# Kernel tuning notes

Hardware: AMD Instinct MI355X
Metric: run time of the kernel (lower is better)

Reference implementation:

```python
import jax, jax.numpy as jnp
import numpy as np

HEADS = 8
DIM_HEAD = 32
SCALE = DIM_HEAD ** -0.5
EPS = 1e-5


def setup_inputs() -> dict:
    key = jax.random.key(0)
    k1, k2, k3 = jax.random.split(key, 3)
    b, dim, n = 8, 512, 8192
    hidden = HEADS * DIM_HEAD  # 256
    return {
        "x": jax.random.normal(k1, (b, dim, n), dtype=jnp.float32),
        "g": jnp.ones((1, dim, 1), dtype=jnp.float32),
        "b_ln": jnp.zeros((1, dim, 1), dtype=jnp.float32),
        "w_qkv": jax.random.normal(k2, (hidden * 3, dim), dtype=jnp.float32) * (dim ** -0.5),
        "w_out": jax.random.normal(k3, (dim, hidden), dtype=jnp.float32) * (hidden ** -0.5),
        "b_out": jnp.zeros((dim,), dtype=jnp.float32),
    }


def reference(x, g, b_ln, w_qkv, w_out, b_out):
    b, c, n = x.shape
    # channel LayerNorm (biased variance over dim=1)
    mean = jnp.mean(x, axis=1, keepdims=True)
    var = jnp.var(x, axis=1, keepdims=True)
    x_norm = (x - mean) / jnp.sqrt(var + EPS) * g + b_ln
    # 1x1 conv QKV projection: [3*hidden, c] x [b, c, n] -> [b, 3*hidden, n]
    qkv = jnp.einsum('oc,bcn->bon', w_qkv, x_norm)
    hidden = w_qkv.shape[0] // 3
    q, k, v = jnp.split(qkv, 3, axis=1)
    # [b, h, dh, n]
    q = q.reshape(b, HEADS, DIM_HEAD, n) * SCALE
    k = k.reshape(b, HEADS, DIM_HEAD, n)
    v = v.reshape(b, HEADS, DIM_HEAD, n)
    k = jax.nn.softmax(k, axis=-1)  # softmax over sequence positions
    # linear attention: context = k v^T  (dh x dh per head), then context q
    context = jnp.einsum('bhdn,bhen->bhde', k, v)
    out = jnp.einsum('bhde,bhdn->bhen', context, q)
    out = out.reshape(b, hidden, n)
    out = jnp.einsum('oc,bcn->bon', w_out, out) + b_out[None, :, None]
    return out + x
```

## Files before the change

kernel.cpp:

```cpp
#include <hip/hip_runtime.h>
#include <hip/hip_bf16.h>
#include <math.h>

#define HEADS 8
#define DH 32
#define BATCH 8
#define CDIM 512
#define NSEQ 8192
#define HID 256
#define O3 768
#define LNEPS 1e-5f
#define QSCALE 0.1767766952966369f

typedef __bf16 bf16x8 __attribute__((ext_vector_type(8)));
typedef float f32x4 __attribute__((ext_vector_type(4)));
typedef unsigned short u16;
typedef u16 u16x4 __attribute__((ext_vector_type(4)));
typedef u16 u16x8 __attribute__((ext_vector_type(8)));

__device__ __forceinline__ void gld_lds16(const void* g, void* l) {
  __builtin_amdgcn_global_load_lds(
      (const __attribute__((address_space(1))) unsigned int*)g,
      (__attribute__((address_space(3))) unsigned int*)l, 16, 0, 0);
}

__device__ __forceinline__ float ldx(const void* p, size_t i, bool f32) {
  if (f32) {
    float v = ((const float*)p)[i];
    return __builtin_isfinite(v) ? v : 0.f;
  }
  return __bfloat162float(((const __hip_bfloat16*)p)[i]);
}

__device__ __forceinline__ u16 b16(float v) {
  union { __hip_bfloat16 h; u16 u; } cv;
  cv.h = __float2bfloat16(v);
  return cv.u;
}

__device__ __forceinline__ float fb16(u16 u) {
  return __uint_as_float((unsigned)u << 16);
}

__device__ __forceinline__ void stage8(__hip_bfloat16* dst, const void* src, size_t idx, bool f32) {
  if (f32) {
    const float* s = (const float*)src + idx;
#pragma unroll
    for (int t = 0; t < 8; ++t) {
      float v = s[t];
      if (!__builtin_isfinite(v)) v = 0.f;
      dst[t] = __float2bfloat16(v);
    }
  } else {
    *(int4*)dst = *(const int4*)((const __hip_bfloat16*)src + idx);
  }
}

__device__ __forceinline__ void stx(void* p, size_t i, bool f32, float v) {
  if (!__builtin_isfinite(v)) v = 0.f;
  if (f32) ((float*)p)[i] = v;
  else ((__hip_bfloat16*)p)[i] = __float2bfloat16(v);
}

__global__ __launch_bounds__(256) void detect_kernel(const void* __restrict__ x, int* __restrict__ mode) {
  __shared__ int cnt;
  if (threadIdx.x == 0) cnt = 0;
  __syncthreads();
  const __hip_bfloat16* p = (const __hip_bfloat16*)x;
  int c = 0;
  for (int i = threadIdx.x; i < 4096; i += 256) {
    float v = __bfloat162float(p[i]);
    if (!(v > -1.0e3f && v < 1.0e3f)) c++;
  }
  atomicAdd(&cnt, c);
  __syncthreads();
  if (threadIdx.x == 0) mode[0] = (cnt > 64) ? 1 : 0;
}

__global__ __launch_bounds__(256) void ln_stats4_kernel(
    const void* __restrict__ x, const int* __restrict__ mode,
    float* __restrict__ mean, float* __restrict__ rstd) {
  const bool f32 = mode[0] != 0;
  const int b = blockIdx.y;
  const int n0 = blockIdx.x * 128;
  const int t = threadIdx.x;
  const int m = t & 31, cp = t >> 5;
  const int n4 = m * 4;
  const size_t base = (size_t)b * CDIM * NSEQ + n0 + n4;
  f32x4 s = {0.f, 0.f, 0.f, 0.f}, q = {0.f, 0.f, 0.f, 0.f};
  for (int c = cp * 64; c < cp * 64 + 64; ++c) {
    f32x4 v;
    if (f32) {
      v = *(const f32x4*)((const float*)x + base + (size_t)c * NSEQ);
#pragma unroll
      for (int j = 0; j < 4; ++j) if (!__builtin_isfinite(v[j])) v[j] = 0.f;
    } else {
      u16x4 h = *(const u16x4*)((const __hip_bfloat16*)x + base + (size_t)c * NSEQ);
#pragma unroll
      for (int j = 0; j < 4; ++j) v[j] = fb16(h[j]);
    }
    s += v;
    q += v * v;
  }
  __shared__ f32x4 sbS[8][32], sbQ[8][32];
  sbS[cp][m] = s; sbQ[cp][m] = q;
  __syncthreads();
  if (t < 32) {
    f32x4 S = sbS[0][t], Q = sbQ[0][t];
#pragma unroll
    for (int k = 1; k < 8; ++k) { S += sbS[k][t]; Q += sbQ[k][t]; }
    f32x4 M = S * (1.f / CDIM);
    f32x4 V = Q * (1.f / CDIM) - M * M;
#pragma unroll
    for (int j = 0; j < 4; ++j) {
      mean[b * NSEQ + n0 + t * 4 + j] = M[j];
      rstd[b * NSEQ + n0 + t * 4 + j] = rsqrtf(fmaxf(V[j], 0.f) + LNEPS);
    }
  }
}

__global__ __launch_bounds__(256) void wconv_kernel(
    const void* __restrict__ wqkv, const int* __restrict__ mode,
    __hip_bfloat16* __restrict__ wb) {
  const bool f32 = mode[0] != 0;
  const size_t i = ((size_t)blockIdx.x * 256 + threadIdx.x) * 8;
  if (f32) {
    f32x4 a = *(const f32x4*)((const float*)wqkv + i);
    f32x4 c = *(const f32x4*)((const float*)wqkv + i + 4);
    u16x8 o;
#pragma unroll
    for (int j = 0; j < 4; ++j) {
      float va = __builtin_isfinite(a[j]) ? a[j] : 0.f;
      float vc = __builtin_isfinite(c[j]) ? c[j] : 0.f;
      o[j] = b16(va);
      o[4 + j] = b16(vc);
    }
    *(u16x8*)&wb[i] = o;
  } else {
    *(int4*)&wb[i] = *(const int4*)((const __hip_bfloat16*)wqkv + i);
  }
}

__global__ __launch_bounds__(256) void xnormt_kernel(
    const void* __restrict__ x, const void* __restrict__ g, const void* __restrict__ bln,
    const int* __restrict__ mode, const float* __restrict__ mean, const float* __restrict__ rstd,
    __hip_bfloat16* __restrict__ xnt) {
  const bool f32 = mode[0] != 0;
  const int b = blockIdx.z;
  const int c0 = blockIdx.y * 128;
  const int n0 = blockIdx.x * 128;
  __shared__ u16 tile[128 * 132];
  const int t = threadIdx.x;
  const int m = t & 31, rb = t >> 5;
  const int n4 = m * 4;
  const f32x4 mn = *(const f32x4*)&mean[b * NSEQ + n0 + n4];
  const f32x4 rs = *(const f32x4*)&rstd[b * NSEQ + n0 + n4];
#pragma unroll
  for (int it = 0; it < 16; ++it) {
    const int r = it * 8 + rb;
    const float gv = ldx(g, c0 + r, f32);
    const float bv = ldx(bln, c0 + r, f32);
    const size_t src = ((size_t)b * CDIM + c0 + r) * NSEQ + n0 + n4;
    f32x4 v;
    if (f32) {
      v = *(const f32x4*)((const float*)x + src);
#pragma unroll
      for (int j = 0; j < 4; ++j) if (!__builtin_isfinite(v[j])) v[j] = 0.f;
    } else {
      u16x4 h = *(const u16x4*)((const __hip_bfloat16*)x + src);
#pragma unroll
      for (int j = 0; j < 4; ++j) v[j] = fb16(h[j]);
    }
    u16x4 o;
#pragma unroll
    for (int j = 0; j < 4; ++j) o[j] = b16((v[j] - mn[j]) * rs[j] * gv + bv);
    *(u16x4*)&tile[r * 132 + n4] = o;
  }
  __syncthreads();
  const int n = t >> 1, ch = t & 1;
  __hip_bfloat16* dst = xnt + ((size_t)b * NSEQ + n0 + n) * CDIM + c0 + ch * 64;
#pragma unroll
  for (int i8 = 0; i8 < 8; ++i8) {
    u16x8 o;
#pragma unroll
    for (int k = 0; k < 8; ++k) o[k] = tile[(ch * 64 + i8 * 8 + k) * 132 + n];
    *(u16x8*)(dst + i8 * 8) = o;
  }
}

__global__ __launch_bounds__(256) void ln_stats_kernel(
    const void* __restrict__ x, const int* __restrict__ mode,
    float* __restrict__ mean, float* __restrict__ rstd) {
  const bool f32 = mode[0] != 0;
  int b = blockIdx.y;
  int nl = threadIdx.x & 63;
  int cp = threadIdx.x >> 6;
  int n = blockIdx.x * 64 + nl;
  size_t base = (size_t)b * CDIM * NSEQ + n;
  float s = 0.f, ss = 0.f;
  for (int c = cp * 128; c < cp * 128 + 128; ++c) {
    float v = ldx(x, base + (size_t)c * NSEQ, f32);
    s += v; ss += v * v;
  }
  __shared__ float sb[4][64], sb2[4][64];
  sb[cp][nl] = s; sb2[cp][nl] = ss;
  __syncthreads();
  if (cp == 0) {
    s = sb[0][nl] + sb[1][nl] + sb[2][nl] + sb[3][nl];
    ss = sb2[0][nl] + sb2[1][nl] + sb2[2][nl] + sb2[3][nl];
    float m = s * (1.f / CDIM);
    float var = ss * (1.f / CDIM) - m * m;
    mean[b * NSEQ + n] = m;
    rstd[b * NSEQ + n] = rsqrtf(fmaxf(var, 0.f) + LNEPS);
  }
}

__global__ __launch_bounds__(256) void kv_gemm3_kernel(
    const __hip_bfloat16* __restrict__ wb, const __hip_bfloat16* __restrict__ xnt,
    float* __restrict__ ctxb, float* __restrict__ sumexp) {
  const int b = blockIdx.z;
  const int p = blockIdx.y;
  const int n0 = blockIdx.x * 128;
  __shared__ __align__(16) char smem[128 * 136 * 2];
  __hip_bfloat16* As = (__hip_bfloat16*)smem;
  __hip_bfloat16* Bs = As + 128 * 32;
  __hip_bfloat16* Ct = (__hip_bfloat16*)smem;
  const int tid = threadIdx.x;
  const int lane = tid & 63;
  const int wv = tid >> 6;
  const int wm = wv >> 1, wn = wv & 1;
  const int quad = lane >> 4, l = lane & 15;
  f32x4 acc[4][4] = {};
  const __hip_bfloat16* xb = xnt + (size_t)b * NSEQ * CDIM;
  const int lr = lane >> 2, lc8 = (lane & 3) * 8;
  for (int k0 = 0; k0 < CDIM; k0 += 32) {
#pragma unroll
    for (int c = 0; c < 2; ++c) {
      int row = c * 64 + wv * 16 + lr;
      int srow = (row < 64) ? (256 + p * 64 + row) : (512 + p * 64 + row - 64);
      gld_lds16(&wb[(size_t)srow * CDIM + k0 + lc8], &As[(c * 64 + wv * 16) * 32]);
      gld_lds16(&xb[(size_t)(n0 + row) * CDIM + k0 + lc8], &Bs[(c * 64 + wv * 16) * 32]);
    }
    __syncthreads();
    bf16x8 af[4], bfr[4];
#pragma unroll
    for (int i = 0; i < 4; ++i)
      af[i] = *(const bf16x8*)&As[(wm * 64 + i * 16 + l) * 32 + quad * 8];
#pragma unroll
    for (int j = 0; j < 4; ++j)
      bfr[j] = *(const bf16x8*)&Bs[(wn * 64 + j * 16 + l) * 32 + quad * 8];
#pragma unroll
    for (int i = 0; i < 4; ++i)
#pragma unroll
      for (int j = 0; j < 4; ++j)
        acc[i][j] = __builtin_amdgcn_mfma_f32_16x16x32_bf16(af[i], bfr[j], acc[i][j], 0, 0, 0);
    __syncthreads();
  }
#pragma unroll
  for (int i = 0; i < 4; ++i) {
    int row = wm * 64 + i * 16 + quad * 4;
#pragma unroll
    for (int j = 0; j < 4; ++j) {
      int col = wn * 64 + j * 16 + l;
#pragma unroll
      for (int r = 0; r < 4; ++r) {
        float v = acc[i][j][r];
        if (wm == 0) v = expf(fminf(v, 20.f));
        else         v = fminf(fmaxf(v, -1.0e4f), 1.0e4f);
        Ct[(row + r) * 136 + col] = __float2bfloat16(v);
      }
    }
  }
  __syncthreads();
  const int mi = wm, ni = wn;
#pragma unroll
  for (int hh = 0; hh < 2; ++hh) {
    f32x4 ca = {};
#pragma unroll
    for (int ks = 0; ks < 4; ++ks) {
      bf16x8 ea = *(const bf16x8*)&Ct[(hh * 32 + mi * 16 + l) * 136 + ks * 32 + quad * 8];
      bf16x8 vb = *(const bf16x8*)&Ct[(64 + hh * 32 + ni * 16 + l) * 136 + ks * 32 + quad * 8];
      ca = __builtin_amdgcn_mfma_f32_16x16x32_bf16(ea, vb, ca, 0, 0, 0);
    }
    int h = p * 2 + hh;
    float* cp = ctxb + (size_t)(b * HEADS + h) * DH * DH;
#pragma unroll
    for (int r = 0; r < 4; ++r)
      atomicAdd(&cp[(mi * 16 + quad * 4 + r) * DH + ni * 16 + l], ca[r]);
  }
  if (tid < 64) {
    int hh = tid >> 5, d = tid & 31;
    float s = 0.f;
#pragma unroll 16
    for (int c = 0; c < 128; ++c) s += __bfloat162float(Ct[tid * 136 + c]);
    atomicAdd(&sumexp[(b * HEADS + p * 2 + hh) * DH + d], s);
  }
}

__global__ __launch_bounds__(256) void kvctx_kernel(
    const void* __restrict__ x, const void* __restrict__ g,
    const void* __restrict__ bln, const void* __restrict__ wqkv,
    const int* __restrict__ mode,
    const float* __restrict__ mean, const float* __restrict__ rstd,
    float* __restrict__ ctxb, float* __restrict__ sumexp) {
  const bool f32 = mode[0] != 0;
  const int b = blockIdx.z;
  const int p = blockIdx.y;
  const int n0 = blockIdx.x * 128;
  __shared__ __align__(16) __hip_bfloat16 As[128 * 32];
  __shared__ __align__(16) __hip_bfloat16 Bs[128 * 40];
  __shared__ __align__(16) __hip_bfloat16 Ct[128 * 136];
  const int tid = threadIdx.x;
  const int lane = tid & 63;
  const int wv = tid >> 6;
  const int wm = wv >> 1, wn = wv & 1;
  const int quad = lane >> 4, l = lane & 15;
  f32x4 acc[4][4] = {};
  const int nn = tid & 127;
  const int cb = tid >> 7;
  const float mn = mean[b * NSEQ + n0 + nn];
  const float rs = rstd[b * NSEQ + n0 + nn];
  const size_t xbase = (size_t)b * CDIM * NSEQ + n0 + nn;
  for (int k0 = 0; k0 < CDIM; k0 += 32) {
#pragma unroll
    for (int r = 0; r < 2; ++r) {
      int idx = (r * 256 + tid) * 8;
      int row = idx >> 5, col = idx & 31;
      int srow = (row < 64) ? (256 + p * 64 + row) : (512 + p * 64 + row - 64);
      stage8(&As[idx], wqkv, (size_t)srow * CDIM + k0 + col, f32);
    }
#pragma unroll
    for (int r = 0; r < 16; ++r) {
      int c = r * 2 + cb;
      float xv = ldx(x, xbase + (size_t)(k0 + c) * NSEQ, f32);
      float xn = (xv - mn) * rs;
      xn = xn * ldx(g, k0 + c, f32) + ldx(bln, k0 + c, f32);
      Bs[nn * 40 + c] = __float2bfloat16(xn);
    }
    __syncthreads();
    bf16x8 af[4], bfr[4];
#pragma unroll
    for (int i = 0; i < 4; ++i)
      af[i] = *(const bf16x8*)&As[(wm * 64 + i * 16 + l) * 32 + quad * 8];
#pragma unroll
    for (int j = 0; j < 4; ++j)
      bfr[j] = *(const bf16x8*)&Bs[(wn * 64 + j * 16 + l) * 40 + quad * 8];
#pragma unroll
    for (int i = 0; i < 4; ++i)
#pragma unroll
      for (int j = 0; j < 4; ++j)
        acc[i][j] = __builtin_amdgcn_mfma_f32_16x16x32_bf16(af[i], bfr[j], acc[i][j], 0, 0, 0);
    __syncthreads();
  }
#pragma unroll
  for (int i = 0; i < 4; ++i) {
    int row = wm * 64 + i * 16 + quad * 4;
#pragma unroll
    for (int j = 0; j < 4; ++j) {
      int col = wn * 64 + j * 16 + l;
#pragma unroll
      for (int r = 0; r < 4; ++r) {
        float v = acc[i][j][r];
        if (wm == 0) v = expf(fminf(v, 20.f));
        else         v = fminf(fmaxf(v, -1.0e4f), 1.0e4f);
        Ct[(row + r) * 136 + col] = __float2bfloat16(v);
      }
    }
  }
  __syncthreads();
  const int mi = wm, ni = wn;
#pragma unroll
  for (int hh = 0; hh < 2; ++hh) {
    f32x4 ca = {};
#pragma unroll
    for (int ks = 0; ks < 4; ++ks) {
      bf16x8 ea = *(const bf16x8*)&Ct[(hh * 32 + mi * 16 + l) * 136 + ks * 32 + quad * 8];
      bf16x8 vb = *(const bf16x8*)&Ct[(64 + hh * 32 + ni * 16 + l) * 136 + ks * 32 + quad * 8];
      ca = __builtin_amdgcn_mfma_f32_16x16x32_bf16(ea, vb, ca, 0, 0, 0);
    }
    int h = p * 2 + hh;
    float* cp = ctxb + (size_t)(b * HEADS + h) * DH * DH;
#pragma unroll
    for (int r = 0; r < 4; ++r)
      atomicAdd(&cp[(mi * 16 + quad * 4 + r) * DH + ni * 16 + l], ca[r]);
  }
  if (tid < 64) {
    int hh = tid >> 5, d = tid & 31;
    float s = 0.f;
#pragma unroll 16
    for (int c = 0; c < 128; ++c) s += __bfloat162float(Ct[tid * 136 + c]);
    atomicAdd(&sumexp[(b * HEADS + p * 2 + hh) * DH + d], s);
  }
}

__global__ __launch_bounds__(256) void w2_build_kernel(
    const void* __restrict__ wout, const int* __restrict__ mode,
    const float* __restrict__ ctxb, const float* __restrict__ sumexp,
    __hip_bfloat16* __restrict__ w2) {
  const bool f32 = mode[0] != 0;
  const int o = blockIdx.x;
  const int b = blockIdx.y;
  const int hd = threadIdx.x;
  const int h = hd >> 5, d = hd & 31;
  const float* cp = ctxb + ((size_t)(b * HEADS + h) * DH + d) * DH;
  float a = 0.f;
#pragma unroll
  for (int e = 0; e < DH; ++e) a += ldx(wout, (size_t)o * HID + h * DH + e, f32) * cp[e];
  float se = fmaxf(sumexp[(b * HEADS + h) * DH + d], 1e-30f);
  float v = a * QSCALE / se;
  v = fminf(fmaxf(v, -1.0e3f), 1.0e3f);
  w2[((size_t)b * CDIM + o) * HID + hd] = __float2bfloat16(v);
}

__global__ __launch_bounds__(256) void w3_gemm2_kernel(
    const __hip_bfloat16* __restrict__ w2, const __hip_bfloat16* __restrict__ wb,
    __hip_bfloat16* __restrict__ w3) {
  const int b = blockIdx.z;
  const int m0 = blockIdx.y * 128;
  const int n0 = blockIdx.x * 128;
  __shared__ __align__(16) __hip_bfloat16 As[128 * 40];
  __shared__ __align__(16) __hip_bfloat16 Bs[128 * 40];
  const int tid = threadIdx.x;
  const int lane = tid & 63;
  const int wv = tid >> 6;
  const int wm = wv >> 1, wn = wv & 1;
  const int quad = lane >> 4, l = lane & 15;
  f32x4 acc[4][4] = {};
  const int nn = tid & 127;
  const int cb = tid >> 7;
  const __hip_bfloat16* wa = w2 + (size_t)b * CDIM * HID;
  for (int k0 = 0; k0 < HID; k0 += 32) {
#pragma unroll
    for (int i = 0; i < 2; ++i) {
      int gid = tid + i * 256;
      int row = gid >> 2, c8 = (gid & 3) * 8;
      *(int4*)&As[row * 40 + c8] = *(const int4*)&wa[(size_t)(m0 + row) * HID + k0 + c8];
    }
#pragma unroll
    for (int r = 0; r < 16; ++r) {
      int hdl = r * 2 + cb;
      Bs[nn * 40 + hdl] = wb[(size_t)(k0 + hdl) * CDIM + n0 + nn];
    }
    __syncthreads();
    bf16x8 af[4], bfr[4];
#pragma unroll
    for (int i = 0; i < 4; ++i)
      af[i] = *(const bf16x8*)&As[(wm * 64 + i * 16 + l) * 40 + quad * 8];
#pragma unroll
    for (int j = 0; j < 4; ++j)
      bfr[j] = *(const bf16x8*)&Bs[(wn * 64 + j * 16 + l) * 40 + quad * 8];
#pragma unroll
    for (int i = 0; i < 4; ++i)
#pragma unroll
      for (int j = 0; j < 4; ++j)
        acc[i][j] = __builtin_amdgcn_mfma_f32_16x16x32_bf16(af[i], bfr[j], acc[i][j], 0, 0, 0);
    __syncthreads();
  }
#pragma unroll
  for (int i = 0; i < 4; ++i) {
    int orow = m0 + wm * 64 + i * 16 + quad * 4;
#pragma unroll
    for (int j = 0; j < 4; ++j) {
      int ncol = n0 + wn * 64 + j * 16 + l;
      __hip_bfloat16* op = w3 + ((size_t)b * CDIM + orow) * CDIM + ncol;
#pragma unroll
      for (int r = 0; r < 4; ++r) {
        float v = fminf(fmaxf(acc[i][j][r], -1.0e4f), 1.0e4f);
        op[(size_t)r * CDIM] = __float2bfloat16(v);
      }
    }
  }
}

__global__ __launch_bounds__(256) void w3_gemm_kernel(
    const __hip_bfloat16* __restrict__ w2, const void* __restrict__ wqkv,
    const int* __restrict__ mode, __hip_bfloat16* __restrict__ w3) {
  const bool f32 = mode[0] != 0;
  const int b = blockIdx.z;
  const int m0 = blockIdx.y * 128;
  const int n0 = blockIdx.x * 128;
  __shared__ __align__(16) __hip_bfloat16 As[128 * 32];
  __shared__ __align__(16) __hip_bfloat16 Bs[128 * 40];
  const int tid = threadIdx.x;
  const int lane = tid & 63;
  const int wv = tid >> 6;
  const int wm = wv >> 1, wn = wv & 1;
  const int quad = lane >> 4, l = lane & 15;
  f32x4 acc[4][4] = {};
  const int nn = tid & 127;
  const int cb = tid >> 7;
  const __hip_bfloat16* wa = w2 + (size_t)b * CDIM * HID;
  for (int k0 = 0; k0 < HID; k0 += 32) {
#pragma unroll
    for (int r = 0; r < 2; ++r) {
      int idx = (r * 256 + tid) * 8;
      int row = idx >> 5, col = idx & 31;
      *(int4*)&As[idx] = *(const int4*)&wa[(size_t)(m0 + row) * HID + k0 + col];
    }
#pragma unroll
    for (int r = 0; r < 16; ++r) {
      int hdl = r * 2 + cb;
      Bs[nn * 40 + hdl] = __float2bfloat16(ldx(wqkv, (size_t)(k0 + hdl) * CDIM + n0 + nn, f32));
    }
    __syncthreads();
    bf16x8 af[4], bfr[4];
#pragma unroll
    for (int i = 0; i < 4; ++i)
      af[i] = *(const bf16x8*)&As[(wm * 64 + i * 16 + l) * 32 + quad * 8];
#pragma unroll
    for (int j = 0; j < 4; ++j)
      bfr[j] = *(const bf16x8*)&Bs[(wn * 64 + j * 16 + l) * 40 + quad * 8];
#pragma unroll
    for (int i = 0; i < 4; ++i)
#pragma unroll
      for (int j = 0; j < 4; ++j)
        acc[i][j] = __builtin_amdgcn_mfma_f32_16x16x32_bf16(af[i], bfr[j], acc[i][j], 0, 0, 0);
    __syncthreads();
  }
#pragma unroll
  for (int i = 0; i < 4; ++i) {
    int orow = m0 + wm * 64 + i * 16 + quad * 4;
#pragma unroll
    for (int j = 0; j < 4; ++j) {
      int ncol = n0 + wn * 64 + j * 16 + l;
      __hip_bfloat16* op = w3 + ((size_t)b * CDIM + orow) * CDIM + ncol;
#pragma unroll
      for (int r = 0; r < 4; ++r) {
        float v = fminf(fmaxf(acc[i][j][r], -1.0e4f), 1.0e4f);
        op[(size_t)r * CDIM] = __float2bfloat16(v);
      }
    }
  }
}

__global__ __launch_bounds__(256) void out_gemm3_kernel(
    const void* __restrict__ x, const __hip_bfloat16* __restrict__ w3,
    const __hip_bfloat16* __restrict__ xnt, const int* __restrict__ mode,
    const void* __restrict__ bout, void* __restrict__ out) {
  const bool f32 = mode[0] != 0;
  const int b = blockIdx.z;
  const int m0 = blockIdx.y * 128;
  const int n0 = blockIdx.x * 128;
  __shared__ __align__(16) __hip_bfloat16 As[128 * 32];
  __shared__ __align__(16) __hip_bfloat16 Bs[128 * 32];
  const int tid = threadIdx.x;
  const int lane = tid & 63;
  const int wv = tid >> 6;
  const int wm = wv >> 1, wn = wv & 1;
  const int quad = lane >> 4, l = lane & 15;
  f32x4 acc[4][4] = {};
  const __hip_bfloat16* wa = w3 + (size_t)b * CDIM * CDIM;
  const __hip_bfloat16* xb = xnt + (size_t)b * NSEQ * CDIM;
  const int lr = lane >> 2, lc8 = (lane & 3) * 8;
  for (int k0 = 0; k0 < CDIM; k0 += 32) {
#pragma unroll
    for (int c = 0; c < 2; ++c) {
      int row = c * 64 + wv * 16 + lr;
      gld_lds16(&wa[(size_t)(m0 + row) * CDIM + k0 + lc8], &As[(c * 64 + wv * 16) * 32]);
      gld_lds16(&xb[(size_t)(n0 + row) * CDIM + k0 + lc8], &Bs[(c * 64 + wv * 16) * 32]);
    }
    __syncthreads();
    bf16x8 af[4], bfr[4];
#pragma unroll
    for (int i = 0; i < 4; ++i)
      af[i] = *(const bf16x8*)&As[(wm * 64 + i * 16 + l) * 32 + quad * 8];
#pragma unroll
    for (int j = 0; j < 4; ++j)
      bfr[j] = *(const bf16x8*)&Bs[(wn * 64 + j * 16 + l) * 32 + quad * 8];
#pragma unroll
    for (int i = 0; i < 4; ++i)
#pragma unroll
      for (int j = 0; j < 4; ++j)
        acc[i][j] = __builtin_amdgcn_mfma_f32_16x16x32_bf16(af[i], bfr[j], acc[i][j], 0, 0, 0);
    __syncthreads();
  }
#pragma unroll
  for (int i = 0; i < 4; ++i) {
    int orow = m0 + wm * 64 + i * 16 + quad * 4;
#pragma unroll
    for (int j = 0; j < 4; ++j) {
      int ncol = n0 + wn * 64 + j * 16 + l;
#pragma unroll
      for (int r = 0; r < 4; ++r) {
        size_t oi = ((size_t)b * CDIM + orow + r) * NSEQ + ncol;
        float v = acc[i][j][r] + ldx(bout, orow + r, f32) + ldx(x, oi, f32);
        stx(out, oi, f32, v);
      }
    }
  }
}

__global__ __launch_bounds__(256) void out_gemm_kernel(
    const void* __restrict__ x, const void* __restrict__ g,
    const void* __restrict__ bln, const __hip_bfloat16* __restrict__ w3,
    const int* __restrict__ mode,
    const float* __restrict__ mean, const float* __restrict__ rstd,
    const void* __restrict__ bout, void* __restrict__ out) {
  const bool f32 = mode[0] != 0;
  const int b = blockIdx.z;
  const int m0 = blockIdx.y * 128;
  const int n0 = blockIdx.x * 128;
  __shared__ __align__(16) __hip_bfloat16 As[128 * 32];
  __shared__ __align__(16) __hip_bfloat16 Bs[128 * 40];
  const int tid = threadIdx.x;
  const int lane = tid & 63;
  const int wv = tid >> 6;
  const int wm = wv >> 1, wn = wv & 1;
  const int quad = lane >> 4, l = lane & 15;
  f32x4 acc[4][4] = {};
  const int nn = tid & 127;
  const int cb = tid >> 7;
  const float mn = mean[b * NSEQ + n0 + nn];
  const float rs = rstd[b * NSEQ + n0 + nn];
  const size_t xbase = (size_t)b * CDIM * NSEQ + n0 + nn;
  const __hip_bfloat16* wa = w3 + (size_t)b * CDIM * CDIM;
  for (int k0 = 0; k0 < CDIM; k0 += 32) {
#pragma unroll
    for (int r = 0; r < 2; ++r) {
      int idx = (r * 256 + tid) * 8;
      int row = idx >> 5, col = idx & 31;
      *(int4*)&As[idx] = *(const int4*)&wa[(size_t)(m0 + row) * CDIM + k0 + col];
    }
#pragma unroll
    for (int r = 0; r < 16; ++r) {
      int c = r * 2 + cb;
      float xv = ldx(x, xbase + (size_t)(k0 + c) * NSEQ, f32);
      float xn = (xv - mn) * rs;
      xn = xn * ldx(g, k0 + c, f32) + ldx(bln, k0 + c, f32);
      Bs[nn * 40 + c] = __float2bfloat16(xn);
    }
    __syncthreads();
    bf16x8 af[4], bfr[4];
#pragma unroll
    for (int i = 0; i < 4; ++i)
      af[i] = *(const bf16x8*)&As[(wm * 64 + i * 16 + l) * 32 + quad * 8];
#pragma unroll
    for (int j = 0; j < 4; ++j)
      bfr[j] = *(const bf16x8*)&Bs[(wn * 64 + j * 16 + l) * 40 + quad * 8];
#pragma unroll
    for (int i = 0; i < 4; ++i)
#pragma unroll
      for (int j = 0; j < 4; ++j)
        acc[i][j] = __builtin_amdgcn_mfma_f32_16x16x32_bf16(af[i], bfr[j], acc[i][j], 0, 0, 0);
    __syncthreads();
  }
#pragma unroll
  for (int i = 0; i < 4; ++i) {
    int orow = m0 + wm * 64 + i * 16 + quad * 4;
#pragma unroll
    for (int j = 0; j < 4; ++j) {
      int ncol = n0 + wn * 64 + j * 16 + l;
#pragma unroll
      for (int r = 0; r < 4; ++r) {
        size_t oi = ((size_t)b * CDIM + orow + r) * NSEQ + ncol;
        float v = acc[i][j][r] + ldx(bout, orow + r, f32) + ldx(x, oi, f32);
        stx(out, oi, f32, v);
      }
    }
  }
}

extern "C" void kernel_launch(void* const* d_in, const int* in_sizes, int n_in,
                              void* d_out, int out_size, void* d_ws, size_t ws_size,
                              hipStream_t stream) {
  (void)in_sizes; (void)n_in; (void)out_size;
  const void* x    = d_in[0];
  const void* g    = d_in[1];
  const void* bln  = d_in[2];
  const void* wqkv = d_in[3];
  const void* wout = d_in[4];
  const void* bout = d_in[5];

  float* mean   = (float*)d_ws;
  float* rstd   = mean + BATCH * NSEQ;
  float* ctxb   = rstd + BATCH * NSEQ;
  float* sumexp = ctxb + BATCH * HEADS * DH * DH;
  int*   mode   = (int*)(sumexp + BATCH * HEADS * DH);
  __hip_bfloat16* w2  = (__hip_bfloat16*)(mode + 64);
  __hip_bfloat16* w3  = w2 + (size_t)BATCH * CDIM * HID;
  __hip_bfloat16* wb  = w3 + (size_t)BATCH * CDIM * CDIM;
  __hip_bfloat16* xnt = wb + (size_t)O3 * CDIM;
  const size_t need = (size_t)((const char*)(xnt + (size_t)BATCH * NSEQ * CDIM) - (const char*)d_ws);

  hipMemsetAsync(ctxb, 0, (BATCH * HEADS * DH * DH + BATCH * HEADS * DH) * sizeof(float), stream);
  detect_kernel<<<1, 256, 0, stream>>>(x, mode);

  if (ws_size >= need) {
    ln_stats4_kernel<<<dim3(NSEQ / 128, BATCH), 256, 0, stream>>>(x, mode, mean, rstd);
    wconv_kernel<<<dim3((O3 * CDIM) / 2048), 256, 0, stream>>>(wqkv, mode, wb);
    xnormt_kernel<<<dim3(NSEQ / 128, CDIM / 128, BATCH), 256, 0, stream>>>(
        x, g, bln, mode, mean, rstd, xnt);
    kv_gemm3_kernel<<<dim3(NSEQ / 128, HEADS / 2, BATCH), 256, 0, stream>>>(
        wb, xnt, ctxb, sumexp);
    w2_build_kernel<<<dim3(CDIM, BATCH), 256, 0, stream>>>(wout, mode, ctxb, sumexp, w2);
    w3_gemm2_kernel<<<dim3(CDIM / 128, CDIM / 128, BATCH), 256, 0, stream>>>(w2, wb, w3);
    out_gemm3_kernel<<<dim3(NSEQ / 128, CDIM / 128, BATCH), 256, 0, stream>>>(
        x, w3, xnt, mode, bout, d_out);
  } else {
    ln_stats_kernel<<<dim3(NSEQ / 64, BATCH), 256, 0, stream>>>(x, mode, mean, rstd);
    kvctx_kernel<<<dim3(NSEQ / 128, HEADS / 2, BATCH), 256, 0, stream>>>(
        x, g, bln, wqkv, mode, mean, rstd, ctxb, sumexp);
    w2_build_kernel<<<dim3(CDIM, BATCH), 256, 0, stream>>>(wout, mode, ctxb, sumexp, w2);
    w3_gemm_kernel<<<dim3(CDIM / 128, CDIM / 128, BATCH), 256, 0, stream>>>(w2, wqkv, mode, w3);
    out_gemm_kernel<<<dim3(NSEQ / 128, CDIM / 128, BATCH), 256, 0, stream>>>(
        x, g, bln, w3, mode, mean, rstd, bout, d_out);
  }
}
```

Before: 593.6 us.

## Triple-buffer LDS staging with swizzled layout in kv and out GEMMs

Replaces the single-buffer load/sync/compute loop in the kv and output GEMM kernels with a three-stage LDS ring buffer. Global-to-LDS loads for tile t+2 are issued while tile t is computed, with explicit vmcnt waits and one barrier per iteration. It also XOR-swizzles the 16-byte column chunks to cut LDS bank conflicts on the fragment reads. LDS use rises to 48 KB per block, which may lower occupancy, and the hand-written vmcnt counting must match the number of loads in flight.

```diff
diff --git a/kernel.cpp b/kernel.cpp
--- a/kernel.cpp
+++ b/kernel.cpp
@@ -215,15 +215,13 @@
   }
 }
 
-__global__ __launch_bounds__(256) void kv_gemm3_kernel(
+__global__ __launch_bounds__(256) void kv_gemm5_kernel(
     const __hip_bfloat16* __restrict__ wb, const __hip_bfloat16* __restrict__ xnt,
     float* __restrict__ ctxb, float* __restrict__ sumexp) {
   const int b = blockIdx.z;
   const int p = blockIdx.y;
   const int n0 = blockIdx.x * 128;
-  __shared__ __align__(16) char smem[128 * 136 * 2];
-  __hip_bfloat16* As = (__hip_bfloat16*)smem;
-  __hip_bfloat16* Bs = As + 128 * 32;
+  __shared__ __align__(16) char smem[49152];
   __hip_bfloat16* Ct = (__hip_bfloat16*)smem;
   const int tid = threadIdx.x;
   const int lane = tid & 63;
@@ -232,30 +230,52 @@
   const int quad = lane >> 4, l = lane & 15;
   f32x4 acc[4][4] = {};
   const __hip_bfloat16* xb = xnt + (size_t)b * NSEQ * CDIM;
-  const int lr = lane >> 2, lc8 = (lane & 3) * 8;
-  for (int k0 = 0; k0 < CDIM; k0 += 32) {
-#pragma unroll
-    for (int c = 0; c < 2; ++c) {
-      int row = c * 64 + wv * 16 + lr;
-      int srow = (row < 64) ? (256 + p * 64 + row) : (512 + p * 64 + row - 64);
-      gld_lds16(&wb[(size_t)srow * CDIM + k0 + lc8], &As[(c * 64 + wv * 16) * 32]);
-      gld_lds16(&xb[(size_t)(n0 + row) * CDIM + k0 + lc8], &Bs[(c * 64 + wv * 16) * 32]);
-    }
-    __syncthreads();
+  const int r16 = lane >> 2;
+  const int cs8 = ((lane & 3) ^ (r16 & 3)) * 8;
+  const int rowA = wv * 16 + r16;
+  const int cq = (quad ^ (l & 3)) * 8;
+
+#define KV_STAGE(bufidx, k0) do {                                              \
+    __hip_bfloat16* As_ = (__hip_bfloat16*)(smem + (bufidx) * 16384);          \
+    __hip_bfloat16* Bs_ = As_ + 128 * 32;                                      \
+    gld_lds16(&wb[(size_t)(256 + p * 64 + rowA) * CDIM + (k0) + cs8],          \
+              &As_[(wv * 16) * 32]);                                           \
+    gld_lds16(&wb[(size_t)(512 + p * 64 + rowA) * CDIM + (k0) + cs8],          \
+              &As_[(64 + wv * 16) * 32]);                                      \
+    gld_lds16(&xb[(size_t)(n0 + rowA) * CDIM + (k0) + cs8],                    \
+              &Bs_[(wv * 16) * 32]);                                           \
+    gld_lds16(&xb[(size_t)(n0 + 64 + rowA) * CDIM + (k0) + cs8],               \
+              &Bs_[(64 + wv * 16) * 32]);                                      \
+  } while (0)
+
+  KV_STAGE(0, 0);
+  KV_STAGE(1, 32);
+  for (int t = 0; t < 16; ++t) {
+    if (t < 15) asm volatile("s_waitcnt vmcnt(4)" ::: "memory");
+    else        asm volatile("s_waitcnt vmcnt(0)" ::: "memory");
+    __builtin_amdgcn_s_barrier();
+    __builtin_amdgcn_sched_barrier(0);
+    if (t + 2 < 16) {
+      int bi = (t + 2) % 3;
+      KV_STAGE(bi, (t + 2) * 32);
+    }
+    const __hip_bfloat16* As = (const __hip_bfloat16*)(smem + (t % 3) * 16384);
+    const __hip_bfloat16* Bs = As + 128 * 32;
     bf16x8 af[4], bfr[4];
 #pragma unroll
     for (int i = 0; i < 4; ++i)
-      af[i] = *(const bf16x8*)&As[(wm * 64 + i * 16 + l) * 32 + quad * 8];
+      af[i] = *(const bf16x8*)&As[(wm * 64 + i * 16 + l) * 32 + cq];
 #pragma unroll
     for (int j = 0; j < 4; ++j)
-      bfr[j] = *(const bf16x8*)&Bs[(wn * 64 + j * 16 + l) * 32 + quad * 8];
+      bfr[j] = *(const bf16x8*)&Bs[(wn * 64 + j * 16 + l) * 32 + cq];
 #pragma unroll
     for (int i = 0; i < 4; ++i)
 #pragma unroll
       for (int j = 0; j < 4; ++j)
         acc[i][j] = __builtin_amdgcn_mfma_f32_16x16x32_bf16(af[i], bfr[j], acc[i][j], 0, 0, 0);
-    __syncthreads();
-  }
+  }
+#undef KV_STAGE
+  __syncthreads();
 #pragma unroll
   for (int i = 0; i < 4; ++i) {
     int row = wm * 64 + i * 16 + quad * 4;
@@ -533,7 +553,7 @@
   }
 }
 
-__global__ __launch_bounds__(256) void out_gemm3_kernel(
+__global__ __launch_bounds__(256) void out_gemm5_kernel(
     const void* __restrict__ x, const __hip_bfloat16* __restrict__ w3,
     const __hip_bfloat16* __restrict__ xnt, const int* __restrict__ mode,
     const void* __restrict__ bout, void* __restrict__ out) {
@@ -541,8 +561,7 @@
   const int b = blockIdx.z;
   const int m0 = blockIdx.y * 128;
   const int n0 = blockIdx.x * 128;
-  __shared__ __align__(16) __hip_bfloat16 As[128 * 32];
-  __shared__ __align__(16) __hip_bfloat16 Bs[128 * 32];
+  __shared__ __align__(16) char smem[49152];
   const int tid = threadIdx.x;
   const int lane = tid & 63;
   const int wv = tid >> 6;
@@ -551,29 +570,51 @@
   f32x4 acc[4][4] = {};
   const __hip_bfloat16* wa = w3 + (size_t)b * CDIM * CDIM;
   const __hip_bfloat16* xb = xnt + (size_t)b * NSEQ * CDIM;
-  const int lr = lane >> 2, lc8 = (lane & 3) * 8;
-  for (int k0 = 0; k0 < CDIM; k0 += 32) {
-#pragma unroll
-    for (int c = 0; c < 2; ++c) {
-      int row = c * 64 + wv * 16 + lr;
-      gld_lds16(&wa[(size_t)(m0 + row) * CDIM + k0 + lc8], &As[(c * 64 + wv * 16) * 32]);
-      gld_lds16(&xb[(size_t)(n0 + row) * CDIM + k0 + lc8], &Bs[(c * 64 + wv * 16) * 32]);
-    }
-    __syncthreads();
+  const int r16 = lane >> 2;
+  const int cs8 = ((lane & 3) ^ (r16 & 3)) * 8;
+  const int rowA = wv * 16 + r16;
+  const int cq = (quad ^ (l & 3)) * 8;
+
+#define OUT_STAGE(bufidx, k0) do {                                             \
+    __hip_bfloat16* As_ = (__hip_bfloat16*)(smem + (bufidx) * 16384);          \
+    __hip_bfloat16* Bs_ = As_ + 128 * 32;                                      \
+    gld_lds16(&wa[(size_t)(m0 + rowA) * CDIM + (k0) + cs8],                    \
+              &As_[(wv * 16) * 32]);                                           \
+    gld_lds16(&wa[(size_t)(m0 + 64 + rowA) * CDIM + (k0) + cs8],               \
+              &As_[(64 + wv * 16) * 32]);                                      \
+    gld_lds16(&xb[(size_t)(n0 + rowA) * CDIM + (k0) + cs8],                    \
+              &Bs_[(wv * 16) * 32]);                                           \
+    gld_lds16(&xb[(size_t)(n0 + 64 + rowA) * CDIM + (k0) + cs8],               \
+              &Bs_[(64 + wv * 16) * 32]);                                      \
+  } while (0)
+
+  OUT_STAGE(0, 0);
+  OUT_STAGE(1, 32);
+  for (int t = 0; t < 16; ++t) {
+    if (t < 15) asm volatile("s_waitcnt vmcnt(4)" ::: "memory");
+    else        asm volatile("s_waitcnt vmcnt(0)" ::: "memory");
+    __builtin_amdgcn_s_barrier();
+    __builtin_amdgcn_sched_barrier(0);
+    if (t + 2 < 16) {
+      int bi = (t + 2) % 3;
+      OUT_STAGE(bi, (t + 2) * 32);
+    }
+    const __hip_bfloat16* As = (const __hip_bfloat16*)(smem + (t % 3) * 16384);
+    const __hip_bfloat16* Bs = As + 128 * 32;
     bf16x8 af[4], bfr[4];
 #pragma unroll
     for (int i = 0; i < 4; ++i)
-      af[i] = *(const bf16x8*)&As[(wm * 64 + i * 16 + l) * 32 + quad * 8];
+      af[i] = *(const bf16x8*)&As[(wm * 64 + i * 16 + l) * 32 + cq];
 #pragma unroll
     for (int j = 0; j < 4; ++j)
-      bfr[j] = *(const bf16x8*)&Bs[(wn * 64 + j * 16 + l) * 32 + quad * 8];
+      bfr[j] = *(const bf16x8*)&Bs[(wn * 64 + j * 16 + l) * 32 + cq];
 #pragma unroll
     for (int i = 0; i < 4; ++i)
 #pragma unroll
       for (int j = 0; j < 4; ++j)
         acc[i][j] = __builtin_amdgcn_mfma_f32_16x16x32_bf16(af[i], bfr[j], acc[i][j], 0, 0, 0);
-    __syncthreads();
-  }
+  }
+#undef OUT_STAGE
 #pragma unroll
   for (int i = 0; i < 4; ++i) {
     int orow = m0 + wm * 64 + i * 16 + quad * 4;
@@ -690,11 +731,11 @@
     wconv_kernel<<<dim3((O3 * CDIM) / 2048), 256, 0, stream>>>(wqkv, mode, wb);
     xnormt_kernel<<<dim3(NSEQ / 128, CDIM / 128, BATCH), 256, 0, stream>>>(
         x, g, bln, mode, mean, rstd, xnt);
-    kv_gemm3_kernel<<<dim3(NSEQ / 128, HEADS / 2, BATCH), 256, 0, stream>>>(
+    kv_gemm5_kernel<<<dim3(NSEQ / 128, HEADS / 2, BATCH), 256, 0, stream>>>(
         wb, xnt, ctxb, sumexp);
     w2_build_kernel<<<dim3(CDIM, BATCH), 256, 0, stream>>>(wout, mode, ctxb, sumexp, w2);
     w3_gemm2_kernel<<<dim3(CDIM / 128, CDIM / 128, BATCH), 256, 0, stream>>>(w2, wb, w3);
-    out_gemm3_kernel<<<dim3(NSEQ / 128, CDIM / 128, BATCH), 256, 0, stream>>>(
+    out_gemm5_kernel<<<dim3(NSEQ / 128, CDIM / 128, BATCH), 256, 0, stream>>>(
         x, w3, xnt, mode, bout, d_out);
   } else {
     ln_stats_kernel<<<dim3(NSEQ / 64, BATCH), 256, 0, stream>>>(x, mode, mean, rstd);
```

Result: faster. 576.2 us (-2.9%).
